# Kernel optimization log

Measured on AMD Instinct MI355X. Metric: run time of the kernel, lower is better.

The kernel has to match this reference:

```python
import jax, jax.numpy as jnp
import numpy as np

B, H, W = 4, 64, 64
DIM, HEADS, HEAD = 768, 12, 64
WIN = 14
MLP_DIM = 4 * DIM
EPS = 1e-5


def _ln(x, g, b):
    mu = jnp.mean(x, axis=-1, keepdims=True)
    var = jnp.mean(jnp.square(x - mu), axis=-1, keepdims=True)
    return (x - mu) * jax.lax.rsqrt(var + EPS) * g + b


def _window_partition(x):
    Bb, Hh, Ww, C = x.shape
    pad_h = (WIN - Hh % WIN) % WIN
    pad_w = (WIN - Ww % WIN) % WIN
    x = jnp.pad(x, ((0, 0), (0, pad_h), (0, pad_w), (0, 0)))
    Hp, Wp = Hh + pad_h, Ww + pad_w
    x = x.reshape(Bb, Hp // WIN, WIN, Wp // WIN, WIN, C)
    win = x.transpose(0, 1, 3, 2, 4, 5).reshape(-1, WIN, WIN, C)
    return win, (Hp, Wp)


def _window_unpartition(win, pad_hw, hw):
    Hp, Wp = pad_hw
    Hh, Ww = hw
    Bb = win.shape[0] // (Hp * Wp // WIN // WIN)
    x = win.reshape(Bb, Hp // WIN, Wp // WIN, WIN, WIN, -1)
    x = x.transpose(0, 1, 3, 2, 4, 5).reshape(Bb, Hp, Wp, -1)
    return x[:, :Hh, :Ww, :]


def _attention(xw, qkv_w, qkv_b, proj_w, proj_b, rel_pos_h, rel_pos_w):
    Bw = xw.shape[0]
    N = WIN * WIN
    qkv = xw.reshape(Bw, N, DIM) @ qkv_w + qkv_b            # [Bw, N, 3*DIM]
    qkv = qkv.reshape(Bw, N, 3, HEADS, HEAD)
    qkv = qkv.transpose(2, 0, 3, 1, 4).reshape(3, Bw * HEADS, N, HEAD)
    q, k, v = qkv[0], qkv[1], qkv[2]
    scale = HEAD ** -0.5
    attn = jnp.einsum('bqc,bkc->bqk', q * scale, k)         # [Bw*HEADS, N, N]
    # decomposed relative position bias (q_size == k_size => plain gather)
    idx = jnp.arange(WIN)[:, None] - jnp.arange(WIN)[None, :] + (WIN - 1)
    Rh = rel_pos_h[idx]
    Rw = rel_pos_w[idx]
    r_q = q.reshape(-1, WIN, WIN, HEAD)
    rel_h = jnp.einsum('bhwc,hkc->bhwk', r_q, Rh)
    rel_w = jnp.einsum('bhwc,wkc->bhwk', r_q, Rw)
    attn = attn.reshape(-1, WIN, WIN, WIN, WIN) + rel_h[..., None] + rel_w[..., None, :]
    attn = jax.nn.softmax(attn.reshape(-1, N, N), axis=-1)
    out = attn @ v                                          # [Bw*HEADS, N, HEAD]
    out = out.reshape(Bw, HEADS, WIN, WIN, HEAD).transpose(0, 2, 3, 1, 4)
    out = out.reshape(Bw, WIN, WIN, DIM)
    return out @ proj_w + proj_b


def setup_inputs() -> dict:
    key = jax.random.key(0)
    ks = jax.random.split(key, 8)
    s = 0.02
    return {
        'x': jax.random.normal(ks[0], (B, H, W, DIM), jnp.float32),
        'norm1_g': jnp.ones((DIM,), jnp.float32),
        'norm1_b': jnp.zeros((DIM,), jnp.float32),
        'qkv_w': jax.random.normal(ks[1], (DIM, 3 * DIM), jnp.float32) * s,
        'qkv_b': jnp.zeros((3 * DIM,), jnp.float32),
        'proj_w': jax.random.normal(ks[2], (DIM, DIM), jnp.float32) * s,
        'proj_b': jnp.zeros((DIM,), jnp.float32),
        'rel_pos_h': jax.random.normal(ks[3], (2 * WIN - 1, HEAD), jnp.float32) * s,
        'rel_pos_w': jax.random.normal(ks[4], (2 * WIN - 1, HEAD), jnp.float32) * s,
        'norm2_g': jnp.ones((DIM,), jnp.float32),
        'norm2_b': jnp.zeros((DIM,), jnp.float32),
        'mlp_w1': jax.random.normal(ks[5], (DIM, MLP_DIM), jnp.float32) * s,
        'mlp_b1': jnp.zeros((MLP_DIM,), jnp.float32),
        'mlp_w2': jax.random.normal(ks[6], (MLP_DIM, DIM), jnp.float32) * s,
        'mlp_b2': jnp.zeros((DIM,), jnp.float32),
    }


def reference(x, norm1_g, norm1_b, qkv_w, qkv_b, proj_w, proj_b,
              rel_pos_h, rel_pos_w, norm2_g, norm2_b,
              mlp_w1, mlp_b1, mlp_w2, mlp_b2):
    shortcut = x
    x = _ln(x, norm1_g, norm1_b)
    win, pad_hw = _window_partition(x)
    win = _attention(win, qkv_w, qkv_b, proj_w, proj_b, rel_pos_h, rel_pos_w)
    x = _window_unpartition(win, pad_hw, (H, W))
    x = shortcut + x
    y = _ln(x, norm2_g, norm2_b)
    y = jax.nn.gelu(y @ mlp_w1 + mlp_b1, approximate=False) @ mlp_w2 + mlp_b2
    return x + y
```

## Files before the change

kernel.cpp:

```cpp
#include <hip/hip_runtime.h>
#include <hip/hip_bf16.h>
#include <math.h>

#define DIMC 768
#define NHEADS 12
#define WINSZ 14
#define NTOK 196
#define TOKENS 16384

using bf = __hip_bfloat16;
typedef __attribute__((ext_vector_type(4))) float f32x4;
typedef __attribute__((ext_vector_type(8))) short bf16x8;

typedef __attribute__((address_space(3))) void lds_void_t;
typedef const __attribute__((address_space(1))) void gmem_void_t;

__device__ inline float bfu2f(ushort u) { return __uint_as_float((uint)u << 16); }
__device__ inline ushort f2bu(float f) {
    bf t = __float2bfloat16(f);
    return __builtin_bit_cast(ushort, t);
}

__global__ __launch_bounds__(256) void transpose_k(const float* __restrict__ in,
                                                   ushort* __restrict__ out, int R, int C) {
    long i = (long)blockIdx.x * 256 + threadIdx.x;
    if (i >= (long)R * C) return;
    int r = (int)(i / C), c = (int)(i % C);
    out[(long)c * R + r] = f2bu(in[i]);
}

__device__ inline float blk_sum(float v, float* wred, int tid) {
    for (int m = 32; m; m >>= 1) v += __shfl_xor(v, m);
    if ((tid & 63) == 0) wred[tid >> 6] = v;
    __syncthreads();
    float r = wred[0] + wred[1] + wred[2] + wred[3];
    __syncthreads();
    return r;
}

__global__ __launch_bounds__(256) void ln_k(const float* __restrict__ x, const float* __restrict__ g,
                                            const float* __restrict__ bb, ushort* __restrict__ out) {
    int row = blockIdx.x, tid = threadIdx.x;
    const float* xr = x + (size_t)row * DIMC;
    __shared__ float wred[4];
    float v0 = xr[tid], v1 = xr[tid + 256], v2 = xr[tid + 512];
    float mean = blk_sum(v0 + v1 + v2, wred, tid) * (1.f / 768.f);
    float d0 = v0 - mean, d1 = v1 - mean, d2 = v2 - mean;
    float var = blk_sum(d0 * d0 + d1 * d1 + d2 * d2, wred, tid) * (1.f / 768.f);
    float rs = rsqrtf(var + 1e-5f);
    ushort* o = out + (size_t)row * DIMC;
    o[tid]       = f2bu(d0 * rs * g[tid]       + bb[tid]);
    o[tid + 256] = f2bu(d1 * rs * g[tid + 256] + bb[tid + 256]);
    o[tid + 512] = f2bu(d2 * rs * g[tid + 512] + bb[tid + 512]);
}

enum { EPI_BIAS = 0, EPI_GELU = 1, EPI_PROJRES = 2, EPI_ACC = 3, EPI_RESOUT = 4 };

template <int EPI>
__global__ __launch_bounds__(256) void gemm_k(const ushort* __restrict__ A, int lda,
                                              const ushort* __restrict__ Bt, int ldb,
                                              const float* __restrict__ bias,
                                              ushort* __restrict__ outb,
                                              float* __restrict__ outf,
                                              const float* __restrict__ xorig,
                                              float* __restrict__ x2,
                                              int N, int K) {
    __shared__ ushort lA0[128 * 32];
    __shared__ ushort lA1[128 * 32];
    __shared__ ushort lB0[128 * 32];
    __shared__ ushort lB1[128 * 32];
    const int bm = blockIdx.y * 128, bn = blockIdx.x * 128;
    const int tid = threadIdx.x, wave = tid >> 6, lane = tid & 63;
    const int wy = wave >> 1, wx = wave & 1;
    const int lm = lane & 15, quad = lane >> 4;

    f32x4 acc[4][4];
#pragma unroll
    for (int r = 0; r < 4; ++r)
#pragma unroll
        for (int s = 0; s < 4; ++s) acc[r][s] = (f32x4){0.f, 0.f, 0.f, 0.f};

    const int c0 = wave * 2, c1 = wave * 2 + 1;
    const int srcg = (lane & 3) ^ ((lane >> 3) & 3);
    const ushort* Ab = A + (size_t)(bm + (lane >> 2)) * lda + srcg * 8;
    const ushort* Bb = Bt + (size_t)(bn + (lane >> 2)) * ldb + srcg * 8;
    const size_t a16 = (size_t)16 * lda, b16 = (size_t)16 * ldb;

    for (int k0 = 0; k0 < K; k0 += 64) {
        __builtin_amdgcn_global_load_lds((gmem_void_t*)(Ab + (size_t)c0 * a16 + k0),
                                         (lds_void_t*)&lA0[c0 * 512], 16, 0, 0);
        __builtin_amdgcn_global_load_lds((gmem_void_t*)(Ab + (size_t)c0 * a16 + k0 + 32),
                                         (lds_void_t*)&lA1[c0 * 512], 16, 0, 0);
        __builtin_amdgcn_global_load_lds((gmem_void_t*)(Ab + (size_t)c1 * a16 + k0),
                                         (lds_void_t*)&lA0[c1 * 512], 16, 0, 0);
        __builtin_amdgcn_global_load_lds((gmem_void_t*)(Ab + (size_t)c1 * a16 + k0 + 32),
                                         (lds_void_t*)&lA1[c1 * 512], 16, 0, 0);
        __builtin_amdgcn_global_load_lds((gmem_void_t*)(Bb + (size_t)c0 * b16 + k0),
                                         (lds_void_t*)&lB0[c0 * 512], 16, 0, 0);
        __builtin_amdgcn_global_load_lds((gmem_void_t*)(Bb + (size_t)c0 * b16 + k0 + 32),
                                         (lds_void_t*)&lB1[c0 * 512], 16, 0, 0);
        __builtin_amdgcn_global_load_lds((gmem_void_t*)(Bb + (size_t)c1 * b16 + k0),
                                         (lds_void_t*)&lB0[c1 * 512], 16, 0, 0);
        __builtin_amdgcn_global_load_lds((gmem_void_t*)(Bb + (size_t)c1 * b16 + k0 + 32),
                                         (lds_void_t*)&lB1[c1 * 512], 16, 0, 0);
        __syncthreads();

        const int rg = (quad ^ ((lm >> 1) & 3)) * 8;
        bf16x8 af0[4], af1[4], bv0[4], bv1[4];
#pragma unroll
        for (int r = 0; r < 4; ++r) {
            af0[r] = *(const bf16x8*)&lA0[(wy * 64 + r * 16 + lm) * 32 + rg];
            af1[r] = *(const bf16x8*)&lA1[(wy * 64 + r * 16 + lm) * 32 + rg];
        }
#pragma unroll
        for (int s = 0; s < 4; ++s) {
            bv0[s] = *(const bf16x8*)&lB0[(wx * 64 + s * 16 + lm) * 32 + rg];
            bv1[s] = *(const bf16x8*)&lB1[(wx * 64 + s * 16 + lm) * 32 + rg];
        }
#pragma unroll
        for (int r = 0; r < 4; ++r)
#pragma unroll
            for (int s = 0; s < 4; ++s) {
                acc[r][s] = __builtin_amdgcn_mfma_f32_16x16x32_bf16(af0[r], bv0[s], acc[r][s], 0, 0, 0);
                acc[r][s] = __builtin_amdgcn_mfma_f32_16x16x32_bf16(af1[r], bv1[s], acc[r][s], 0, 0, 0);
            }
        __syncthreads();
    }

#pragma unroll
    for (int s = 0; s < 4; ++s) {
        int col = bn + wx * 64 + s * 16 + lm;
        float bvl = (EPI == EPI_ACC) ? 0.f : bias[col];
#pragma unroll
        for (int r = 0; r < 4; ++r) {
#pragma unroll
            for (int i = 0; i < 4; ++i) {
                int row = bm + wy * 64 + r * 16 + quad * 4 + i;
                float v = acc[r][s][i] + bvl;
                size_t idx = (size_t)row * N + col;
                if constexpr (EPI == EPI_BIAS) {
                    outb[idx] = f2bu(v);
                } else if constexpr (EPI == EPI_GELU) {
                    outb[idx] = f2bu(0.5f * v * (1.f + erff(v * 0.70710678118f)));
                } else if constexpr (EPI == EPI_PROJRES) {
                    x2[idx] = xorig[idx] + v;
                } else if constexpr (EPI == EPI_ACC) {
                    x2[idx] += v;
                } else {
                    outf[idx] = x2[idx] + v;
                }
            }
        }
    }
}

__global__ __launch_bounds__(256) void attn_k(const ushort* __restrict__ qkv,
                                              const float* __restrict__ qkvb,
                                              const float* __restrict__ relh,
                                              const float* __restrict__ relw,
                                              ushort* __restrict__ aout) {
    const int win = blockIdx.x / NHEADS, head = blockIdx.x % NHEADS;
    const int b = win / 25, wi = win % 25, wr = wi / 5, wc = wi % 5;
    const int hmax = (wr == 4) ? 8 : WINSZ, wmax = (wc == 4) ? 8 : WINSZ;
    const int hoff = head * 64;
    const int tid = threadIdx.x, wave = tid >> 6, lane = tid & 63;
    const int c = lane & 15, quad = lane >> 4;

    __shared__ ushort Ksw[224 * 64];
    __shared__ ushort vTs[64 * 264];
    __shared__ ushort wscr[4][640];

    for (int t = tid; t < 224 * 8; t += 256) {
        int n = t >> 3, ck = t & 7;
        int kh = n >> 4, kw = n & 15;
        uint4 vals;
        if (kw < WINSZ && kh < hmax && kw < wmax) {
            size_t tok = ((size_t)(b * 64 + wr * WINSZ + kh) * 64 + wc * WINSZ + kw);
            vals = *(const uint4*)(qkv + tok * 2304 + 768 + hoff + ck * 8);
        } else if (kw < WINSZ) {
            union { uint4 u; ushort s[8]; } tmp;
#pragma unroll
            for (int j = 0; j < 8; ++j) tmp.s[j] = f2bu(qkvb[768 + hoff + ck * 8 + j]);
            vals = tmp.u;
        } else {
            vals = (uint4){0u, 0u, 0u, 0u};
        }
        *(uint4*)&Ksw[n * 64 + ((ck ^ (n & 7)) * 8)] = vals;
    }
    for (int t = tid; t < 224 * 8; t += 256) {
        int n = t >> 3, dg = t & 7;
        int kh = n >> 4, kw = n & 15;
        union { uint4 u; ushort s[8]; } vals;
        if (kw < WINSZ && kh < hmax && kw < wmax) {
            size_t tok = ((size_t)(b * 64 + wr * WINSZ + kh) * 64 + wc * WINSZ + kw);
            vals.u = *(const uint4*)(qkv + tok * 2304 + 1536 + hoff + dg * 8);
        } else if (kw < WINSZ) {
#pragma unroll
            for (int j = 0; j < 8; ++j) vals.s[j] = f2bu(qkvb[1536 + hoff + dg * 8 + j]);
        } else {
            vals.u = (uint4){0u, 0u, 0u, 0u};
        }
        int kchunk = n >> 3;
#pragma unroll
        for (int j = 0; j < 8; ++j) {
            int d = dg * 8 + j;
            vTs[d * 264 + ((kchunk ^ dg) * 8) + (n & 7)] = vals.s[j];
        }
    }
    __syncthreads();

    bf16x8 rhB[2][2], rwB[2][2];
#pragma unroll
    for (int nt = 0; nt < 2; ++nt) {
        int j = nt * 16 + c; if (j > 26) j = 26;
#pragma unroll
        for (int ks = 0; ks < 2; ++ks) {
            const float* ph = relh + (size_t)j * 64 + ks * 32 + quad * 8;
            const float* pw = relw + (size_t)j * 64 + ks * 32 + quad * 8;
            bf16x8 h, w;
#pragma unroll
            for (int e = 0; e < 8; ++e) {
                h[e] = (short)f2bu(ph[e]);
                w[e] = (short)f2bu(pw[e]);
            }
            rhB[nt][ks] = h; rwB[nt][ks] = w;
        }
    }

    ushort* scr = &wscr[wave][0];
    const int lane48 = lane & 48;

    for (int qh = wave; qh < hmax; qh += 4) {
        int qw = c < wmax ? c : (wmax - 1);
        size_t qtok = ((size_t)(b * 64 + wr * WINSZ + qh) * 64 + wc * WINSZ + qw);
        bf16x8 aq0 = *(const bf16x8*)(qkv + qtok * 2304 + hoff + quad * 8);
        bf16x8 aq1 = *(const bf16x8*)(qkv + qtok * 2304 + hoff + 32 + quad * 8);

        f32x4 z = (f32x4){0.f, 0.f, 0.f, 0.f};
        f32x4 dh0 = __builtin_amdgcn_mfma_f32_16x16x32_bf16(aq0, rhB[0][0], z, 0, 0, 0);
        dh0 = __builtin_amdgcn_mfma_f32_16x16x32_bf16(aq1, rhB[0][1], dh0, 0, 0, 0);
        f32x4 dh1 = __builtin_amdgcn_mfma_f32_16x16x32_bf16(aq0, rhB[1][0], z, 0, 0, 0);
        dh1 = __builtin_amdgcn_mfma_f32_16x16x32_bf16(aq1, rhB[1][1], dh1, 0, 0, 0);
        f32x4 dw0 = __builtin_amdgcn_mfma_f32_16x16x32_bf16(aq0, rwB[0][0], z, 0, 0, 0);
        dw0 = __builtin_amdgcn_mfma_f32_16x16x32_bf16(aq1, rwB[0][1], dw0, 0, 0, 0);
        f32x4 dw1 = __builtin_amdgcn_mfma_f32_16x16x32_bf16(aq0, rwB[1][0], z, 0, 0, 0);
        dw1 = __builtin_amdgcn_mfma_f32_16x16x32_bf16(aq1, rwB[1][1], dw1, 0, 0, 0);

#pragma unroll
        for (int i = 0; i < 4; ++i) {
            scr[(quad * 4 + i) * 28 + c] = f2bu(dh0[i]);
            if (c < 12) scr[(quad * 4 + i) * 28 + 16 + c] = f2bu(dh1[i]);
        }

        float bw[4];
#pragma unroll
        for (int i = 0; i < 4; ++i) {
            int m = quad * 4 + i;
            int j = m - c + 13; int jc = j < 0 ? 0 : j;
            int addr = (lane48 | (jc & 15)) << 2;
            int t0 = __builtin_amdgcn_ds_bpermute(addr, __float_as_int(dw0[i]));
            int t1 = __builtin_amdgcn_ds_bpermute(addr, __float_as_int(dw1[i]));
            bw[i] = (jc >= 16) ? __int_as_float(t1) : __int_as_float(t0);
        }

        f32x4 s[14];
#pragma unroll
        for (int kh = 0; kh < 14; ++kh) {
            int n = kh * 16 + c;
            int n7 = n & 7;
            bf16x8 kb0 = *(const bf16x8*)&Ksw[n * 64 + ((0 * 4 + quad) ^ n7) * 8];
            bf16x8 kb1 = *(const bf16x8*)&Ksw[n * 64 + ((1 * 4 + quad) ^ n7) * 8];
            f32x4 acc = __builtin_amdgcn_mfma_f32_16x16x32_bf16(aq0, kb0, z, 0, 0, 0);
            acc = __builtin_amdgcn_mfma_f32_16x16x32_bf16(aq1, kb1, acc, 0, 0, 0);
            int jstar = qh + 13 - kh;
#pragma unroll
            for (int i = 0; i < 4; ++i) {
                float dh = bfu2f(scr[(quad * 4 + i) * 28 + jstar]);
                float v = fmaf(0.125f, acc[i], dh + bw[i]);
                acc[i] = (c < WINSZ) ? v : -1e30f;
            }
            s[kh] = acc;
        }

        float inv[4];
#pragma unroll
        for (int i = 0; i < 4; ++i) {
            float mx = s[0][i];
#pragma unroll
            for (int kh = 1; kh < 14; ++kh) mx = fmaxf(mx, s[kh][i]);
            mx = fmaxf(mx, __shfl_xor(mx, 1));
            mx = fmaxf(mx, __shfl_xor(mx, 2));
            mx = fmaxf(mx, __shfl_xor(mx, 4));
            mx = fmaxf(mx, __shfl_xor(mx, 8));
            float sum = 0.f;
#pragma unroll
            for (int kh = 0; kh < 14; ++kh) {
                float e = __expf(s[kh][i] - mx);
                s[kh][i] = e;
                sum += e;
            }
            sum += __shfl_xor(sum, 1);
            sum += __shfl_xor(sum, 2);
            sum += __shfl_xor(sum, 4);
            sum += __shfl_xor(sum, 8);
            inv[i] = 1.f / sum;
        }

        f32x4 o[4] = {z, z, z, z};
#pragma unroll
        for (int cc = 0; cc < 7; ++cc) {
#pragma unroll
            for (int i = 0; i < 4; ++i) {
                scr[(quad * 4 + i) * 40 + c]      = f2bu(s[2 * cc][i] * inv[i]);
                scr[(quad * 4 + i) * 40 + 16 + c] = f2bu(s[2 * cc + 1][i] * inv[i]);
            }
            bf16x8 ap = *(const bf16x8*)&scr[c * 40 + quad * 8];
#pragma unroll
            for (int vt = 0; vt < 4; ++vt) {
                int d = vt * 16 + c;
                int dgr = (d >> 3) & 7;
                bf16x8 vb = *(const bf16x8*)&vTs[d * 264 + (((cc * 4 + quad) ^ dgr) * 8)];
                o[vt] = __builtin_amdgcn_mfma_f32_16x16x32_bf16(ap, vb, o[vt], 0, 0, 0);
            }
        }

#pragma unroll
        for (int i = 0; i < 4; ++i) {
            int qwp = quad * 4 + i;
            if (qwp < wmax) {
                size_t otok = ((size_t)(b * 64 + wr * WINSZ + qh) * 64 + wc * WINSZ + qwp);
#pragma unroll
                for (int vt = 0; vt < 4; ++vt)
                    aout[otok * 768 + hoff + vt * 16 + c] = f2bu(o[vt][i]);
            }
        }
    }
}

extern "C" void kernel_launch(void* const* d_in, const int* in_sizes, int n_in,
                              void* d_out, int out_size, void* d_ws, size_t ws_size,
                              hipStream_t stream) {
    const float* x      = (const float*)d_in[0];
    const float* n1g    = (const float*)d_in[1];
    const float* n1b    = (const float*)d_in[2];
    const float* qkv_w  = (const float*)d_in[3];
    const float* qkv_b  = (const float*)d_in[4];
    const float* proj_w = (const float*)d_in[5];
    const float* proj_b = (const float*)d_in[6];
    const float* relh   = (const float*)d_in[7];
    const float* relw   = (const float*)d_in[8];
    const float* n2g    = (const float*)d_in[9];
    const float* n2b    = (const float*)d_in[10];
    const float* w1     = (const float*)d_in[11];
    const float* b1     = (const float*)d_in[12];
    const float* w2     = (const float*)d_in[13];
    const float* b2     = (const float*)d_in[14];
    float* out = (float*)d_out;

    char* ws = (char*)d_ws;
    size_t off = 0;
    auto alloc = [&](size_t bytes) -> void* {
        void* p = ws + off;
        off += (bytes + 255) & ~(size_t)255;
        return p;
    };

    ushort* lnbuf  = (ushort*)alloc((size_t)TOKENS * DIMC * 2);
    ushort* qkvbuf = (ushort*)alloc((size_t)TOKENS * 2304 * 2);
    float* x2      = (float*)alloc((size_t)TOKENS * DIMC * 4);
    ushort* qkvT   = (ushort*)alloc((size_t)2304 * 768 * 2);
    ushort* projT  = (ushort*)alloc((size_t)768 * 768 * 2);
    ushort* w1T    = (ushort*)alloc((size_t)3072 * 768 * 2);
    ushort* w2T    = (ushort*)alloc((size_t)768 * 3072 * 2);
    ushort* aout   = lnbuf;
    ushort* hc     = qkvbuf;

    transpose_k<<<(768 * 2304 + 255) / 256, 256, 0, stream>>>(qkv_w, qkvT, 768, 2304);
    transpose_k<<<(768 * 768 + 255) / 256, 256, 0, stream>>>(proj_w, projT, 768, 768);
    transpose_k<<<(768 * 3072 + 255) / 256, 256, 0, stream>>>(w1, w1T, 768, 3072);
    transpose_k<<<(3072 * 768 + 255) / 256, 256, 0, stream>>>(w2, w2T, 3072, 768);

    ln_k<<<TOKENS, 256, 0, stream>>>(x, n1g, n1b, lnbuf);

    dim3 gq(2304 / 128, TOKENS / 128);
    gemm_k<EPI_BIAS><<<gq, 256, 0, stream>>>(lnbuf, DIMC, qkvT, DIMC, qkv_b, qkvbuf,
                                             nullptr, nullptr, nullptr, 2304, DIMC);

    attn_k<<<100 * NHEADS, 256, 0, stream>>>(qkvbuf, qkv_b, relh, relw, aout);

    dim3 gp(DIMC / 128, TOKENS / 128);
    gemm_k<EPI_PROJRES><<<gp, 256, 0, stream>>>(aout, DIMC, projT, DIMC, proj_b, nullptr,
                                                nullptr, x, x2, DIMC, DIMC);

    ln_k<<<TOKENS, 256, 0, stream>>>(x2, n2g, n2b, lnbuf);

    dim3 gh(1536 / 128, TOKENS / 128);
    for (int c = 0; c < 2; ++c) {
        gemm_k<EPI_GELU><<<gh, 256, 0, stream>>>(lnbuf, DIMC, w1T + (size_t)c * 1536 * 768, DIMC,
                                                 b1 + c * 1536, hc, nullptr, nullptr, nullptr,
                                                 1536, DIMC);
        if (c == 0)
            gemm_k<EPI_ACC><<<gp, 256, 0, stream>>>(hc, 1536, w2T + (size_t)c * 1536, 3072,
                                                    b2, nullptr, nullptr, nullptr, x2, DIMC, 1536);
        else
            gemm_k<EPI_RESOUT><<<gp, 256, 0, stream>>>(hc, 1536, w2T + (size_t)c * 1536, 3072,
                                                       b2, nullptr, out, nullptr, x2, DIMC, 1536);
    }
}
```

Before: 701.8 us.

## Double-buffer GEMM LDS tiles and swizzle block order across XCDs

The GEMM kernel now keeps two LDS buffers per operand and issues global-to-LDS loads for the next K-tile before computing on the current one. This is meant to overlap memory latency with MFMA work. Block indices are also remapped in groups of eight so that neighbouring tiles share L2 on the same die. The cost is double the LDS use per block, which may reduce occupancy. The remap also assumes the grid size divides evenly by eight.

Result: faster. 678.7 us (-3.3%).

```diff
diff --git a/kernel.cpp b/kernel.cpp
--- a/kernel.cpp
+++ b/kernel.cpp
@@ -65,11 +65,17 @@
                                               const float* __restrict__ xorig,
                                               float* __restrict__ x2,
                                               int N, int K) {
-    __shared__ ushort lA0[128 * 32];
-    __shared__ ushort lA1[128 * 32];
-    __shared__ ushort lB0[128 * 32];
-    __shared__ ushort lB1[128 * 32];
-    const int bm = blockIdx.y * 128, bn = blockIdx.x * 128;
+    __shared__ ushort lA0[2][128 * 32];
+    __shared__ ushort lA1[2][128 * 32];
+    __shared__ ushort lB0[2][128 * 32];
+    __shared__ ushort lB1[2][128 * 32];
+
+    const int nwg = gridDim.x * gridDim.y;
+    const int l = blockIdx.y * gridDim.x + blockIdx.x;
+    const int nl = (l & 7) * (nwg >> 3) + (l >> 3);
+    const int bx = nl % gridDim.x, by = nl / gridDim.x;
+    const int bm = by * 128, bn = bx * 128;
+
     const int tid = threadIdx.x, wave = tid >> 6, lane = tid & 63;
     const int wy = wave >> 1, wx = wave & 1;
     const int lm = lane & 15, quad = lane >> 4;
@@ -86,36 +92,45 @@
     const ushort* Bb = Bt + (size_t)(bn + (lane >> 2)) * ldb + srcg * 8;
     const size_t a16 = (size_t)16 * lda, b16 = (size_t)16 * ldb;
 
-    for (int k0 = 0; k0 < K; k0 += 64) {
+    auto stage = [&](int bi, int k0) {
         __builtin_amdgcn_global_load_lds((gmem_void_t*)(Ab + (size_t)c0 * a16 + k0),
-                                         (lds_void_t*)&lA0[c0 * 512], 16, 0, 0);
+                                         (lds_void_t*)&lA0[bi][c0 * 512], 16, 0, 0);
         __builtin_amdgcn_global_load_lds((gmem_void_t*)(Ab + (size_t)c0 * a16 + k0 + 32),
-                                         (lds_void_t*)&lA1[c0 * 512], 16, 0, 0);
+                                         (lds_void_t*)&lA1[bi][c0 * 512], 16, 0, 0);
         __builtin_amdgcn_global_load_lds((gmem_void_t*)(Ab + (size_t)c1 * a16 + k0),
-                                         (lds_void_t*)&lA0[c1 * 512], 16, 0, 0);
+                                         (lds_void_t*)&lA0[bi][c1 * 512], 16, 0, 0);
         __builtin_amdgcn_global_load_lds((gmem_void_t*)(Ab + (size_t)c1 * a16 + k0 + 32),
-                                         (lds_void_t*)&lA1[c1 * 512], 16, 0, 0);
+                                         (lds_void_t*)&lA1[bi][c1 * 512], 16, 0, 0);
         __builtin_amdgcn_global_load_lds((gmem_void_t*)(Bb + (size_t)c0 * b16 + k0),
-                                         (lds_void_t*)&lB0[c0 * 512], 16, 0, 0);
+                                         (lds_void_t*)&lB0[bi][c0 * 512], 16, 0, 0);
         __builtin_amdgcn_global_load_lds((gmem_void_t*)(Bb + (size_t)c0 * b16 + k0 + 32),
-                                         (lds_void_t*)&lB1[c0 * 512], 16, 0, 0);
+                                         (lds_void_t*)&lB1[bi][c0 * 512], 16, 0, 0);
         __builtin_amdgcn_global_load_lds((gmem_void_t*)(Bb + (size_t)c1 * b16 + k0),
-                                         (lds_void_t*)&lB0[c1 * 512], 16, 0, 0);
+                                         (lds_void_t*)&lB0[bi][c1 * 512], 16, 0, 0);
         __builtin_amdgcn_global_load_lds((gmem_void_t*)(Bb + (size_t)c1 * b16 + k0 + 32),
-                                         (lds_void_t*)&lB1[c1 * 512], 16, 0, 0);
-        __syncthreads();
-
-        const int rg = (quad ^ ((lm >> 1) & 3)) * 8;
+                                         (lds_void_t*)&lB1[bi][c1 * 512], 16, 0, 0);
+    };
+
+    const int rg = (quad ^ ((lm >> 1) & 3)) * 8;
+    const int nt = K >> 6;
+
+    stage(0, 0);
+    __syncthreads();
+
+    for (int t = 0; t < nt; ++t) {
+        const int cur = t & 1;
+        if (t + 1 < nt) stage(cur ^ 1, (t + 1) * 64);
+
         bf16x8 af0[4], af1[4], bv0[4], bv1[4];
 #pragma unroll
         for (int r = 0; r < 4; ++r) {
-            af0[r] = *(const bf16x8*)&lA0[(wy * 64 + r * 16 + lm) * 32 + rg];
-            af1[r] = *(const bf16x8*)&lA1[(wy * 64 + r * 16 + lm) * 32 + rg];
+            af0[r] = *(const bf16x8*)&lA0[cur][(wy * 64 + r * 16 + lm) * 32 + rg];
+            af1[r] = *(const bf16x8*)&lA1[cur][(wy * 64 + r * 16 + lm) * 32 + rg];
         }
 #pragma unroll
         for (int s = 0; s < 4; ++s) {
-            bv0[s] = *(const bf16x8*)&lB0[(wx * 64 + s * 16 + lm) * 32 + rg];
-            bv1[s] = *(const bf16x8*)&lB1[(wx * 64 + s * 16 + lm) * 32 + rg];
+            bv0[s] = *(const bf16x8*)&lB0[cur][(wx * 64 + s * 16 + lm) * 32 + rg];
+            bv1[s] = *(const bf16x8*)&lB1[cur][(wx * 64 + s * 16 + lm) * 32 + rg];
         }
 #pragma unroll
         for (int r = 0; r < 4; ++r)
```
